# Performance work log

Hardware: AMD Instinct MI355X
Metric: run time of the kernel (lower is better)

Reference implementation:

```python
import jax, jax.numpy as jnp
import numpy as np

F_DIM = 128
N_RBF = 20
CUTOFF = 5.0
N_LAYERS = 3
EPS = 1e-8


def setup_inputs() -> dict:
    key = jax.random.key(0)
    ks = jax.random.split(key, 16)
    N, E = 10000, 320000
    atomic_numbers = jax.random.randint(ks[0], (N,), 0, 100)
    r_ij = jax.random.normal(ks[1], (E, 3), dtype=jnp.float32)
    idx_i = jnp.sort(jax.random.randint(ks[2], (E,), 0, N))
    idx_j = jax.random.randint(ks[3], (E,), 0, N)
    emb = jax.random.normal(ks[4], (100, F_DIM), dtype=jnp.float32)
    emb = emb.at[0].set(0.0)  # padding_idx=0
    s = 0.05
    return {
        "atomic_numbers": atomic_numbers,
        "r_ij": r_ij,
        "idx_i": idx_i,
        "idx_j": idx_j,
        "embedding": emb,
        "filt_W": jax.random.normal(ks[5], (N_RBF, N_LAYERS * 3 * F_DIM), dtype=jnp.float32) * s,
        "filt_b": jax.random.normal(ks[6], (N_LAYERS * 3 * F_DIM,), dtype=jnp.float32) * s,
        "int_W1": jax.random.normal(ks[7], (N_LAYERS, F_DIM, F_DIM), dtype=jnp.float32) * s,
        "int_b1": jax.random.normal(ks[8], (N_LAYERS, F_DIM), dtype=jnp.float32) * s,
        "int_W2": jax.random.normal(ks[9], (N_LAYERS, F_DIM, 3 * F_DIM), dtype=jnp.float32) * s,
        "int_b2": jax.random.normal(ks[10], (N_LAYERS, 3 * F_DIM), dtype=jnp.float32) * s,
        "mix_W1": jax.random.normal(ks[11], (N_LAYERS, 2 * F_DIM, F_DIM), dtype=jnp.float32) * s,
        "mix_b1": jax.random.normal(ks[12], (N_LAYERS, F_DIM), dtype=jnp.float32) * s,
        "mix_W2": jax.random.normal(ks[13], (N_LAYERS, F_DIM, 3 * F_DIM), dtype=jnp.float32) * s,
        "mix_b2": jax.random.normal(ks[14], (N_LAYERS, 3 * F_DIM), dtype=jnp.float32) * s,
        "mux_W": jax.random.normal(ks[15], (N_LAYERS, F_DIM, 2 * F_DIM), dtype=jnp.float32) * s,
    }


def _painn(embedding, filt_W, filt_b, int_W1, int_b1, int_W2, int_b2,
           mix_W1, mix_b1, mix_W2, mix_b2, mux_W,
           r_ij, atomic_numbers, idx_i, idx_j):
    N = atomic_numbers.shape[0]
    F = F_DIM
    d_ij = jnp.linalg.norm(r_ij, axis=1, keepdims=True)          # [E,1]
    dir_ij = r_ij / d_ij                                          # [E,3]
    # Gaussian RBF expansion
    offset = jnp.linspace(0.0, CUTOFF, N_RBF, dtype=jnp.float32)
    coeff = -0.5 / (offset[1] - offset[0]) ** 2
    phi = jnp.exp(coeff * (d_ij[..., None] - offset) ** 2)        # [E,1,n_rbf]
    # Cosine cutoff
    fcut = 0.5 * (jnp.cos(d_ij * jnp.pi / CUTOFF) + 1.0) * (d_ij < CUTOFF)  # [E,1]
    filters = (phi @ filt_W + filt_b) * fcut[..., None]           # [E,1,L*3F]
    filter_list = jnp.split(filters, N_LAYERS, axis=-1)

    q = embedding[atomic_numbers][:, None, :]                     # [N,1,F]
    mu = jnp.zeros((N, 3, F), dtype=q.dtype)

    for i in range(N_LAYERS):
        Wij = filter_list[i]                                      # [E,1,3F]
        # interaction
        h = jax.nn.silu(q @ int_W1[i] + int_b1[i])
        x = h @ int_W2[i] + int_b2[i]                             # [N,1,3F]
        xj = x[idx_j]                                             # [E,1,3F]
        muj = mu[idx_j]                                           # [E,3,F]
        xw = Wij * xj
        dq, dmuR, dmumu = jnp.split(xw, 3, axis=-1)               # each [E,1,F]
        dq = jax.ops.segment_sum(dq, idx_i, num_segments=N)       # [N,1,F]
        dmu = dmuR * dir_ij[:, :, None] + dmumu * muj             # [E,3,F]
        dmu = jax.ops.segment_sum(dmu, idx_i, num_segments=N)     # [N,3,F]
        q = q + dq
        mu = mu + dmu
        # mixing
        mu_mix = mu @ mux_W[i]                                    # [N,3,2F]
        mu_V, mu_W = jnp.split(mu_mix, 2, axis=-1)
        mu_Vn = jnp.sqrt(jnp.sum(mu_V ** 2, axis=-2, keepdims=True) + EPS)  # [N,1,F]
        ctx = jnp.concatenate([q, mu_Vn], axis=-1)                # [N,1,2F]
        h = jax.nn.silu(ctx @ mix_W1[i] + mix_b1[i])
        x = h @ mix_W2[i] + mix_b2[i]                             # [N,1,3F]
        dq_i, dmu_i, dqmu_i = jnp.split(x, 3, axis=-1)
        dmu_i = dmu_i * mu_W                                      # [N,3,F]
        dqmu_i = dqmu_i * jnp.sum(mu_V * mu_W, axis=1, keepdims=True)
        q = q + dq_i + dqmu_i
        mu = mu + dmu_i
    return q[:, 0, :], mu


def reference(atomic_numbers, r_ij, idx_i, idx_j, embedding, filt_W, filt_b,
              int_W1, int_b1, int_W2, int_b2, mix_W1, mix_b1, mix_W2, mix_b2, mux_W):
    return _painn(embedding, filt_W, filt_b, int_W1, int_b1, int_W2, int_b2,
                  mix_W1, mix_b1, mix_W2, mix_b2, mux_W,
                  r_ij, atomic_numbers, idx_i, idx_j)
```

## Files before the change

kernel.cpp:

```cpp
#include <hip/hip_runtime.h>
#include <hip/hip_bf16.h>
#include <hip/hip_fp16.h>

#define F_DIM 128
#define N_RBF 20
#define CUTOFF 5.0f
#define PI_F 3.14159265358979323846f
#define NPB 4

typedef float v2f __attribute__((ext_vector_type(2)));
typedef __attribute__((ext_vector_type(8))) short bf16x8;
typedef __attribute__((ext_vector_type(4))) float f32x4;
typedef _Float16 h2f __attribute__((ext_vector_type(2)));
typedef _Float16 f16x8 __attribute__((ext_vector_type(8)));

__device__ __forceinline__ unsigned int bf16_rtne(float f) {
    unsigned int u = __float_as_uint(f);
    u += 0x7fffu + ((u >> 16) & 1u);
    return u >> 16;
}
__device__ __forceinline__ unsigned int pack_bf2(float lo, float hi) {
    return bf16_rtne(lo) | (bf16_rtne(hi) << 16);
}
__device__ __forceinline__ float unpk_lo(unsigned int u) {
    return __uint_as_float(u << 16);
}
__device__ __forceinline__ float unpk_hi(unsigned int u) {
    return __uint_as_float(u & 0xffff0000u);
}
__device__ __forceinline__ float bf16_to_f(unsigned short s) {
    return __uint_as_float(((unsigned int)s) << 16);
}
__device__ __forceinline__ unsigned int pack_h2(float lo, float hi) {
    h2f h = (h2f){(_Float16)lo, (_Float16)hi};
    return __builtin_bit_cast(unsigned int, h);
}
__device__ __forceinline__ unsigned short f16_bits(float f) {
    _Float16 h = (_Float16)f;
    return __builtin_bit_cast(unsigned short, h);
}
__device__ __forceinline__ float f16_to_f(unsigned short s) {
    return (float)__builtin_bit_cast(_Float16, s);
}

__global__ __launch_bounds__(256) void k_pre(
        const int* __restrict__ idx_i, int* __restrict__ row_ptr,
        const float* __restrict__ r, unsigned int* __restrict__ geom,
        const float* __restrict__ muxW,
        const float* __restrict__ W1,
        const float* __restrict__ W2,
        const float* __restrict__ iW1,
        const float* __restrict__ iW2,
        const float* __restrict__ filt_W,
        const float* __restrict__ filt_b,
        unsigned short* __restrict__ muxWt,
        unsigned short* __restrict__ W1t,
        unsigned short* __restrict__ W2t,
        unsigned short* __restrict__ iW1t,
        unsigned short* __restrict__ iW2t,
        unsigned short* __restrict__ filtWt,
        int N, int E, int nbR, int nbG) {
    int bid = blockIdx.x;
    if (bid < nbR) {
        int i = bid * 256 + threadIdx.x;
        if (i > N) return;
        if (i == N) { row_ptr[N] = E; return; }
        int lo = 0, hi = E;
        while (lo < hi) {
            int mid = (lo + hi) >> 1;
            if (idx_i[mid] < i) lo = mid + 1; else hi = mid;
        }
        row_ptr[i] = lo;
        return;
    }
    if (bid < nbR + nbG) {
        int e = (bid - nbR) * 256 + threadIdx.x;
        if (e >= E) return;
        float x = r[e * 3], y = r[e * 3 + 1], z = r[e * 3 + 2];
        float d = sqrtf(x * x + y * y + z * z);
        float inv = 1.f / d;
        float fc = (d < CUTOFF) ? 0.5f * (__cosf(d * (PI_F / CUTOFF)) + 1.f) : 0.f;
        unsigned int* g = geom + (size_t)e * 16;
        float dx = x * inv, dy = y * inv, dz = z * inv;
        g[0] = __float_as_uint(dx);
        g[1] = __float_as_uint(dy);
        g[2] = __float_as_uint(dz);
        g[3] = __float_as_uint(fc);
        const float delta = CUTOFF / (N_RBF - 1);
        const float coeff = -0.5f / (delta * delta);
        float ph[N_RBF];
#pragma unroll
        for (int k = 0; k < N_RBF; k++) {
            float t = d - k * delta;
            ph[k] = __expf(coeff * t * t) * fc;
        }
#pragma unroll
        for (int k = 0; k < N_RBF / 2; k++)
            g[4 + k] = pack_h2(ph[2 * k], ph[2 * k + 1]);
        g[14] = pack_h2(fc, dx);
        g[15] = pack_h2(dy, dz);
        return;
    }
    int idx = (bid - nbR - nbG) * 256 + threadIdx.x;
    if (idx < 98304) {
        int l = idx / 32768, rem = idx % 32768;
        int c = rem / 128, k = rem % 128;
        muxWt[idx] = (unsigned short)bf16_rtne(muxW[l * 32768 + k * 256 + c]);
    } else if (idx < 196608) {
        int i2 = idx - 98304;
        int l = i2 / 32768, rem = i2 % 32768;
        int c = rem / 256, k = rem % 256;
        W1t[i2] = (unsigned short)bf16_rtne(W1[l * 32768 + k * 128 + c]);
    } else if (idx < 344064) {
        int i2 = idx - 196608;
        int l = i2 / 49152, rem = i2 % 49152;
        int c = rem / 128, k = rem % 128;
        W2t[i2] = (unsigned short)bf16_rtne(W2[l * 49152 + k * 384 + c]);
    } else if (idx < 393216) {
        int i2 = idx - 344064;
        int l = i2 / 16384, rem = i2 % 16384;
        int c = rem / 128, k = rem % 128;
        iW1t[i2] = (unsigned short)bf16_rtne(iW1[l * 16384 + k * 128 + c]);
    } else if (idx < 540672) {
        int i2 = idx - 393216;
        int l = i2 / 49152, rem = i2 % 49152;
        int c = rem / 128, k = rem % 128;
        iW2t[i2] = (unsigned short)bf16_rtne(iW2[l * 49152 + k * 384 + c]);
    } else if (idx < 568320) {
        int i2 = idx - 540672;
        int l = i2 / 9216, rem = i2 % 9216;
        int c = rem / 24, k = rem % 24;
        float v = 0.f;
        if (k < 20)       v = filt_W[k * 1152 + l * 384 + c];
        else if (k == 20) v = filt_b[l * 384 + c];
        _Float16 hv = (_Float16)v;
        filtWt[i2] = __builtin_bit_cast(unsigned short, hv);
    }
}

__global__ __launch_bounds__(256) void k_node_mfma(
        const int* __restrict__ Z,
        const float* __restrict__ emb,
        float* __restrict__ q,
        const unsigned short* __restrict__ iW1t,
        const float* __restrict__ b1,
        const unsigned short* __restrict__ iW2t,
        const float* __restrict__ b2,
        unsigned int* __restrict__ P, int N) {
    __shared__ unsigned short A[16 * 136];
    __shared__ unsigned short Ah[16 * 136];
    __shared__ float Xs[16 * 396];
    int t = threadIdx.x;
    int w = t >> 6, l = t & 63, quad = l >> 4, c0 = l & 15;
    int n0 = blockIdx.x * 16;

#pragma unroll
    for (int i = 0; i < 4; i++) {
        int flat = i * 256 + t;
        int node = flat >> 6, cp = flat & 63;
        int gn = n0 + node;
        unsigned int v = 0u;
        if (gn < N) {
            const float* s = emb + (size_t)Z[gn] * 128 + 2 * cp;
            float s0 = s[0], s1 = s[1];
            v = pack_bf2(s0, s1);
            float* qo = q + (size_t)gn * 128 + 2 * cp;
            qo[0] = s0; qo[1] = s1;
        }
        *(unsigned int*)&A[node * 136 + 2 * cp] = v;
    }
    __syncthreads();

    bf16x8 a1[4];
#pragma unroll
    for (int ks = 0; ks < 4; ks++)
        a1[ks] = *(const bf16x8*)&A[c0 * 136 + ks * 32 + quad * 8];
#pragma unroll
    for (int jj = 0; jj < 2; jj++) {
        int jg = 2 * w + jj;
        float bb = b1[16 * jg + c0];
        f32x4 acc = (f32x4){bb, bb, bb, bb};
#pragma unroll
        for (int ks = 0; ks < 4; ks++) {
            bf16x8 b = *(const bf16x8*)&iW1t[(16 * jg + c0) * 128 + ks * 32 + quad * 8];
            acc = __builtin_amdgcn_mfma_f32_16x16x32_bf16(a1[ks], b, acc, 0, 0, 0);
        }
#pragma unroll
        for (int r = 0; r < 4; r++) {
            float aa = acc[r];
            Ah[(quad * 4 + r) * 136 + 16 * jg + c0] =
                (unsigned short)bf16_rtne(aa / (1.f + __expf(-aa)));
        }
    }
    __syncthreads();

    bf16x8 a3[4];
#pragma unroll
    for (int ks = 0; ks < 4; ks++)
        a3[ks] = *(const bf16x8*)&Ah[c0 * 136 + ks * 32 + quad * 8];
#pragma unroll
    for (int jj = 0; jj < 6; jj++) {
        int jx = 6 * w + jj;
        float bb = b2[16 * jx + c0];
        f32x4 acc = (f32x4){bb, bb, bb, bb};
#pragma unroll
        for (int ks = 0; ks < 4; ks++) {
            bf16x8 b = *(const bf16x8*)&iW2t[(16 * jx + c0) * 128 + ks * 32 + quad * 8];
            acc = __builtin_amdgcn_mfma_f32_16x16x32_bf16(a3[ks], b, acc, 0, 0, 0);
        }
#pragma unroll
        for (int r = 0; r < 4; r++)
            Xs[(quad * 4 + r) * 396 + 16 * jx + c0] = acc[r];
    }
    __syncthreads();

    int n = t >> 4, fi = (t & 15) * 8;
    int gn = n0 + n;
    if (gn < N) {
        size_t base = (size_t)gn * 384;
        unsigned int d[8];
#pragma unroll
        for (int k = 0; k < 8; k++) {
            float x0 = Xs[n * 396 + fi + k];
            float x1 = Xs[n * 396 + 128 + fi + k];
            float x2 = Xs[n * 396 + 256 + fi + k];
            d[k] = pack_bf2(x0, x1);
            ((unsigned short*)&P[base + 256 + fi + k])[0] = (unsigned short)bf16_rtne(x2);
        }
        *(uint4*)&P[base + fi]     = make_uint4(d[0], d[1], d[2], d[3]);
        *(uint4*)&P[base + fi + 4] = make_uint4(d[4], d[5], d[6], d[7]);
    }
}

__device__ __forceinline__ f16x8 load_phi_frag(const unsigned int* __restrict__ geom,
                                               int ts, int c0, int quad, int E) {
    int ea = ts + c0;
    if (ea >= E) ea = E - 1;
    f16x8 a = {};
    if (quad < 3)
        a = *(const f16x8*)&geom[(size_t)ea * 16 + 4 + quad * 4];
    return a;
}

template <bool HAS_MU>
__global__ __launch_bounds__(256, 8) void k_edge(
        const unsigned int* __restrict__ P,
        const unsigned int* __restrict__ geom,
        const int* __restrict__ idx_j,
        const int* __restrict__ row_ptr,
        const unsigned short* __restrict__ filtWt,
        float* __restrict__ q,
        float* __restrict__ muD, int N, int E) {
    constexpr int NT = HAS_MU ? 6 : 4;
    constexpr int WS = HAS_MU ? 412 : 268;
    __shared__ unsigned short Ws[16 * WS];
    __shared__ float red[4][128];
    int t = threadIdx.x;
    int f = t & 127;
    int sub = __builtin_amdgcn_readfirstlane(t >> 7);
    int w = t >> 6, l = t & 63, quad = l >> 4, c0 = l & 15;

    f16x8 Bf[NT];
#pragma unroll
    for (int jj = 0; jj < NT; jj++) {
        int jx = NT * w + jj;
        f16x8 b = {};
        if (quad < 3)
            b = *(const f16x8*)&filtWt[(16 * jx + c0) * 24 + quad * 8];
        Bf[jj] = b;
    }

    int i0 = blockIdx.x * NPB;
    for (int nn = 0; nn < NPB; nn++) {
        int i = i0 + nn;
        if (i >= N) break;
        int rs = __builtin_amdgcn_readfirstlane(row_ptr[i]);
        int re = __builtin_amdgcn_readfirstlane(row_ptr[i + 1]);
        float dq = 0.f;
        v2f dm01 = (v2f){0.f, 0.f};
        float dm2 = 0.f;

        f16x8 a = load_phi_frag(geom, rs, c0, quad, E);
        for (int ts = rs; ts < re; ts += 16) {
#pragma unroll
            for (int jj = 0; jj < NT; jj++) {
                int jx = NT * w + jj;
                f32x4 acc = (f32x4){0.f, 0.f, 0.f, 0.f};
                acc = __builtin_amdgcn_mfma_f32_16x16x32_f16(a, Bf[jj], acc, 0, 0, 0);
#pragma unroll
                for (int r = 0; r < 4; r++)
                    Ws[(quad * 4 + r) * WS + 16 * jx + c0] = f16_bits(acc[r]);
            }
            __syncthreads();
            if (ts + 16 < re) a = load_phi_frag(geom, ts + 16, c0, quad, E);

            int te = (re < ts + 16) ? re : ts + 16;
            for (int e = ts + sub; e < te; e += 2) {
                int j = __builtin_amdgcn_readfirstlane(idx_j[e]);
                const unsigned int* Pj = P + (size_t)j * 384;
                unsigned int A = Pj[f];
                unsigned int B = 0, C = 0;
                if (HAS_MU) { B = Pj[128 + f]; C = Pj[256 + f]; }

                const float* g = (const float*)(geom + (size_t)e * 16);
                float dirx = g[0], diry = g[1], dirz = g[2];

                int eloc = e - ts;
                float wq = f16_to_f(Ws[eloc * WS + f]);
                float wr = f16_to_f(Ws[eloc * WS + 128 + f]);

                float xq = unpk_lo(A), xr = unpk_hi(A);
                dq += wq * xq;
                float s_r = wr * xr;
                if (HAS_MU) {
                    float wm = f16_to_f(Ws[eloc * WS + 256 + f]);
                    float xm = unpk_lo(C);
                    float s_m = wm * xm;
                    dm01 += (v2f){s_r, s_r} * (v2f){dirx, diry} +
                            (v2f){s_m, s_m} * (v2f){unpk_lo(B), unpk_hi(B)};
                    dm2  += s_r * dirz + s_m * unpk_hi(C);
                } else {
                    dm01 += (v2f){s_r, s_r} * (v2f){dirx, diry};
                    dm2  += s_r * dirz;
                }
            }
            __syncthreads();
        }

        if (sub == 1) { red[0][f] = dq; red[1][f] = dm01.x; red[2][f] = dm01.y; red[3][f] = dm2; }
        __syncthreads();
        if (sub == 0) {
            dq += red[0][f];
            float d0 = dm01.x + red[1][f], d1 = dm01.y + red[2][f];
            dm2 += red[3][f];
            q[(size_t)i * 128 + f] += dq;
            size_t base = (size_t)i * 384;
            if (HAS_MU) {
                muD[base + f]       += d0;
                muD[base + 128 + f] += d1;
                muD[base + 256 + f] += dm2;
            } else {
                muD[base + f]       = d0;
                muD[base + 128 + f] = d1;
                muD[base + 256 + f] = dm2;
            }
        }
        __syncthreads();
    }
}

__global__ __launch_bounds__(256, 3) void k_mix_fused(
        float* __restrict__ q, float* __restrict__ mu,
        const unsigned short* __restrict__ muxWt,
        const unsigned short* __restrict__ W1t,
        const unsigned short* __restrict__ W2t,
        const float* __restrict__ b1,
        const float* __restrict__ b2,
        const unsigned short* __restrict__ niW1t,
        const float* __restrict__ nib1,
        const unsigned short* __restrict__ niW2t,
        const float* __restrict__ nib2,
        int has_node,
        unsigned int* __restrict__ P, int N) {
    constexpr int XS = 516;
    __shared__ __align__(16) unsigned char LDSm[54144];
    unsigned short* A   = (unsigned short*)LDSm;
    unsigned short* Wsp = (unsigned short*)(LDSm + 8448);
    float*          Xs  = (float*)(LDSm + 21120);
    unsigned short* Amu = (unsigned short*)(LDSm + 21120);

    int t = threadIdx.x;
    int w = t >> 6, l = t & 63, quad = l >> 4, c0 = l & 15;
    int n0 = blockIdx.x * 16;

#pragma unroll
    for (int i = 0; i < 4; i++) {
        int flat = i * 256 + t;
        int node = flat >> 6, cp = flat & 63, gn = n0 + node;
        unsigned int v = 0u;
        if (gn < N) { const float* s = q + (size_t)gn * 128 + 2 * cp; v = pack_bf2(s[0], s[1]); }
        *(unsigned int*)&A[node * 264 + 2 * cp] = v;
    }
#pragma unroll
    for (int i = 0; i < 12; i++) {
        int flat = i * 256 + t;
        int row = flat >> 6, cp = flat & 63;
        int node = row & 15, c = row >> 4, gn = n0 + node;
        unsigned int v = 0u;
        if (gn < N) {
            const float* s = mu + (size_t)gn * 384 + c * 128 + 2 * cp;
            v = pack_bf2(s[0], s[1]);
        }
        *(unsigned int*)&Amu[row * 136 + 2 * cp] = v;
    }
    __syncthreads();

    f32x4 vn2[2], S[2];
#pragma unroll
    for (int jj = 0; jj < 2; jj++) { vn2[jj] = (f32x4){0,0,0,0}; S[jj] = (f32x4){0,0,0,0}; }
#pragma unroll
    for (int rt = 0; rt < 3; rt++) {
        bf16x8 af[4];
#pragma unroll
        for (int ks = 0; ks < 4; ks++)
            af[ks] = *(const bf16x8*)&Amu[(rt * 16 + c0) * 136 + ks * 32 + quad * 8];
#pragma unroll
        for (int jj = 0; jj < 2; jj++) {
            int jv = 2 * w + jj;
            f32x4 V = (f32x4){0,0,0,0}, Wm = (f32x4){0,0,0,0};
#pragma unroll
            for (int ks = 0; ks < 4; ks++) {
                bf16x8 bV = *(const bf16x8*)&muxWt[(16 * jv + c0) * 128 + ks * 32 + quad * 8];
                V = __builtin_amdgcn_mfma_f32_16x16x32_bf16(af[ks], bV, V, 0, 0, 0);
            }
#pragma unroll
            for (int ks = 0; ks < 4; ks++) {
                bf16x8 bW = *(const bf16x8*)&muxWt[(16 * (jv + 8) + c0) * 128 + ks * 32 + quad * 8];
                Wm = __builtin_amdgcn_mfma_f32_16x16x32_bf16(af[ks], bW, Wm, 0, 0, 0);
            }
            vn2[jj] += V * V;
            S[jj]   += V * Wm;
#pragma unroll
            for (int r = 0; r < 4; r++)
                Wsp[rt * 2112 + (quad * 4 + r) * 132 + 16 * jv + c0] =
                    (unsigned short)bf16_rtne(Wm[r]);
        }
    }
#pragma unroll
    for (int jj = 0; jj < 2; jj++) {
        int jv = 2 * w + jj;
#pragma unroll
        for (int r = 0; r < 4; r++)
            A[(quad * 4 + r) * 264 + 128 + 16 * jv + c0] =
                (unsigned short)bf16_rtne(sqrtf(vn2[jj][r] + 1e-8f));
    }
    __syncthreads();

    bf16x8 a2[8];
#pragma unroll
    for (int ks = 0; ks < 8; ks++)
        a2[ks] = *(const bf16x8*)&A[c0 * 264 + ks * 32 + quad * 8];
    {
        unsigned short htmp[2][4];
#pragma unroll
        for (int jj = 0; jj < 2; jj++) {
            int jg = 2 * w + jj;
            float bb = b1[16 * jg + c0];
            f32x4 acc = (f32x4){bb, bb, bb, bb};
#pragma unroll
            for (int ks = 0; ks < 8; ks++) {
                bf16x8 b = *(const bf16x8*)&W1t[(16 * jg + c0) * 256 + ks * 32 + quad * 8];
                acc = __builtin_amdgcn_mfma_f32_16x16x32_bf16(a2[ks], b, acc, 0, 0, 0);
            }
#pragma unroll
            for (int r = 0; r < 4; r++) {
                float aa = acc[r];
                htmp[jj][r] = (unsigned short)bf16_rtne(aa / (1.f + __expf(-aa)));
            }
        }
        __syncthreads();
#pragma unroll
        for (int jj = 0; jj < 2; jj++) {
            int jg = 2 * w + jj;
#pragma unroll
            for (int r = 0; r < 4; r++)
                A[(quad * 4 + r) * 264 + 128 + 16 * jg + c0] = htmp[jj][r];
        }
    }
    __syncthreads();

    bf16x8 a3[4];
#pragma unroll
    for (int ks = 0; ks < 4; ks++)
        a3[ks] = *(const bf16x8*)&A[c0 * 264 + 128 + ks * 32 + quad * 8];
#pragma unroll
    for (int jj = 0; jj < 6; jj++) {
        int jx = 6 * w + jj;
        float bb = b2[16 * jx + c0];
        f32x4 acc = (f32x4){bb, bb, bb, bb};
#pragma unroll
        for (int ks = 0; ks < 4; ks++) {
            bf16x8 b = *(const bf16x8*)&W2t[(16 * jx + c0) * 128 + ks * 32 + quad * 8];
            acc = __builtin_amdgcn_mfma_f32_16x16x32_bf16(a3[ks], b, acc, 0, 0, 0);
        }
#pragma unroll
        for (int r = 0; r < 4; r++)
            Xs[(quad * 4 + r) * XS + 16 * jx + c0] = acc[r];
    }
#pragma unroll
    for (int jj = 0; jj < 2; jj++) {
        int jv = 2 * w + jj;
#pragma unroll
        for (int r = 0; r < 4; r++)
            Xs[(quad * 4 + r) * XS + 388 + 16 * jv + c0] = S[jj][r];
    }
    __syncthreads();

    int n = t >> 4, fi = (t & 15) * 8;
    int gn = n0 + n;
    if (gn < N) {
        float* qp = q + (size_t)gn * 128 + fi;
        float qn[8];
#pragma unroll
        for (int k = 0; k < 8; k++) {
            qn[k] = qp[k] + Xs[n * XS + fi + k] +
                    Xs[n * XS + 256 + fi + k] * Xs[n * XS + 388 + fi + k];
            qp[k] = qn[k];
        }
        unsigned int qd[4];
#pragma unroll
        for (int p = 0; p < 4; p++) qd[p] = pack_bf2(qn[2 * p], qn[2 * p + 1]);
        *(uint4*)&A[n * 264 + fi] = make_uint4(qd[0], qd[1], qd[2], qd[3]);

        size_t base = (size_t)gn * 384;
        float m[3][8];
#pragma unroll
        for (int c = 0; c < 3; c++) {
            float* mp = mu + base + c * 128 + fi;
#pragma unroll
            for (int k = 0; k < 8; k++) {
                m[c][k] = mp[k] + Xs[n * XS + 128 + fi + k] *
                                  bf16_to_f(Wsp[c * 2112 + n * 132 + fi + k]);
                mp[k] = m[c][k];
            }
        }
        unsigned int d[8];
#pragma unroll
        for (int k = 0; k < 8; k++) {
            d[k] = pack_bf2(m[0][k], m[1][k]);
            ((unsigned short*)&P[base + 256 + fi + k])[1] = (unsigned short)bf16_rtne(m[2][k]);
        }
        *(uint4*)&P[base + 128 + fi]     = make_uint4(d[0], d[1], d[2], d[3]);
        *(uint4*)&P[base + 128 + fi + 4] = make_uint4(d[4], d[5], d[6], d[7]);
    }
    __syncthreads();

    if (has_node) {
        unsigned short* Ah = Wsp;
        bf16x8 a1[4];
#pragma unroll
        for (int ks = 0; ks < 4; ks++)
            a1[ks] = *(const bf16x8*)&A[c0 * 264 + ks * 32 + quad * 8];
#pragma unroll
        for (int jj = 0; jj < 2; jj++) {
            int jg = 2 * w + jj;
            float bb = nib1[16 * jg + c0];
            f32x4 acc = (f32x4){bb, bb, bb, bb};
#pragma unroll
            for (int ks = 0; ks < 4; ks++) {
                bf16x8 b = *(const bf16x8*)&niW1t[(16 * jg + c0) * 128 + ks * 32 + quad * 8];
                acc = __builtin_amdgcn_mfma_f32_16x16x32_bf16(a1[ks], b, acc, 0, 0, 0);
            }
#pragma unroll
            for (int r = 0; r < 4; r++) {
                float aa = acc[r];
                Ah[(quad * 4 + r) * 136 + 16 * jg + c0] =
                    (unsigned short)bf16_rtne(aa / (1.f + __expf(-aa)));
            }
        }
        __syncthreads();

        bf16x8 a4[4];
#pragma unroll
        for (int ks = 0; ks < 4; ks++)
            a4[ks] = *(const bf16x8*)&Ah[c0 * 136 + ks * 32 + quad * 8];
#pragma unroll
        for (int jj = 0; jj < 6; jj++) {
            int jx = 6 * w + jj;
            float bb = nib2[16 * jx + c0];
            f32x4 acc = (f32x4){bb, bb, bb, bb};
#pragma unroll
            for (int ks = 0; ks < 4; ks++) {
                bf16x8 b = *(const bf16x8*)&niW2t[(16 * jx + c0) * 128 + ks * 32 + quad * 8];
                acc = __builtin_amdgcn_mfma_f32_16x16x32_bf16(a4[ks], b, acc, 0, 0, 0);
            }
#pragma unroll
            for (int r = 0; r < 4; r++)
                Xs[(quad * 4 + r) * XS + 16 * jx + c0] = acc[r];
        }
        __syncthreads();

        if (gn < N) {
            size_t base = (size_t)gn * 384;
            unsigned int d[8];
#pragma unroll
            for (int k = 0; k < 8; k++) {
                float x0 = Xs[n * XS + fi + k];
                float x1 = Xs[n * XS + 128 + fi + k];
                float x2 = Xs[n * XS + 256 + fi + k];
                d[k] = pack_bf2(x0, x1);
                ((unsigned short*)&P[base + 256 + fi + k])[0] = (unsigned short)bf16_rtne(x2);
            }
            *(uint4*)&P[base + fi]     = make_uint4(d[0], d[1], d[2], d[3]);
            *(uint4*)&P[base + fi + 4] = make_uint4(d[4], d[5], d[6], d[7]);
        }
    }
}

extern "C" void kernel_launch(void* const* d_in, const int* in_sizes, int n_in,
                              void* d_out, int out_size, void* d_ws, size_t ws_size,
                              hipStream_t stream) {
    const int*   Z      = (const int*)d_in[0];
    const float* r_ij   = (const float*)d_in[1];
    const int*   idx_i  = (const int*)d_in[2];
    const int*   idx_j  = (const int*)d_in[3];
    const float* emb    = (const float*)d_in[4];
    const float* filt_W = (const float*)d_in[5];
    const float* filt_b = (const float*)d_in[6];
    const float* int_W1 = (const float*)d_in[7];
    const float* int_b1 = (const float*)d_in[8];
    const float* int_W2 = (const float*)d_in[9];
    const float* int_b2 = (const float*)d_in[10];
    const float* mix_W1 = (const float*)d_in[11];
    const float* mix_b1 = (const float*)d_in[12];
    const float* mix_W2 = (const float*)d_in[13];
    const float* mix_b2 = (const float*)d_in[14];
    const float* mux_W  = (const float*)d_in[15];

    int N = in_sizes[0];
    int E = in_sizes[2];

    float* q   = (float*)d_out;
    float* muD = q + (size_t)N * 128;

    unsigned int* geom = (unsigned int*)d_ws;
    unsigned int* P = geom + (size_t)E * 16;
    int* row_ptr = (int*)(P + (size_t)N * 384);
    uintptr_t waddr = (uintptr_t)(row_ptr + N + 1);
    waddr = (waddr + 15) & ~(uintptr_t)15;
    unsigned short* muxWt = (unsigned short*)waddr;
    unsigned short* W1t   = muxWt + 98304;
    unsigned short* W2t   = W1t + 98304;
    unsigned short* iW1t  = W2t + 147456;
    unsigned short* iW2t  = iW1t + 49152;
    unsigned short* filtWt = iW2t + 147456;

    int nbR = (N + 1 + 255) / 256;
    int nbG = (E + 255) / 256;
    k_pre<<<nbR + nbG + 2220, 256, 0, stream>>>(
        idx_i, row_ptr, r_ij, geom,
        mux_W, mix_W1, mix_W2, int_W1, int_W2, filt_W, filt_b,
        muxWt, W1t, W2t, iW1t, iW2t, filtWt, N, E, nbR, nbG);

    int tiles = (N + 15) / 16;
    k_node_mfma<<<tiles, 256, 0, stream>>>(
        Z, emb, q, iW1t, int_b1, iW2t, int_b2, P, N);
    for (int l = 0; l < 3; l++) {
        if (l == 0)
            k_edge<false><<<(N + NPB - 1) / NPB, 256, 0, stream>>>(
                P, geom, idx_j, row_ptr, filtWt, q, muD, N, E);
        else
            k_edge<true><<<(N + NPB - 1) / NPB, 256, 0, stream>>>(
                P, geom, idx_j, row_ptr, filtWt + (size_t)l * 9216, q, muD, N, E);
        int nl = (l < 2) ? (l + 1) : 0;
        k_mix_fused<<<tiles, 256, 0, stream>>>(
            q, muD, muxWt + (size_t)l * 32768, W1t + (size_t)l * 32768,
            W2t + (size_t)l * 49152, mix_b1 + l * 128, mix_b2 + l * 384,
            iW1t + (size_t)nl * 16384, int_b1 + nl * 128,
            iW2t + (size_t)nl * 49152, int_b2 + nl * 384,
            (l < 2) ? 1 : 0, P, N);
    }
}
```

Measured before the change: 532.6 us.

## Prefetch next edge tile's neighbor features into registers in edge kernel

The edge kernel now loads the idx_j values for a whole 16-edge tile with one vector load and broadcasts them with readlane. The neighbor rows of P for the next tile are gathered into registers while the current tile is being processed, so those gathers overlap with compute. The inner edge loop is fully unrolled over 8 slots with masking instead of a variable-trip loop. Occupancy bound drops from 8 to 6 to make room for the extra registers, and the mix kernel skips writing packed mu into P on the last layer where it is no longer read.

After: 880.6 us. 1.65x slower.

```diff
diff --git a/kernel.cpp b/kernel.cpp
--- a/kernel.cpp
+++ b/kernel.cpp
@@ -243,7 +243,7 @@
 }
 
 template <bool HAS_MU>
-__global__ __launch_bounds__(256, 8) void k_edge(
+__global__ __launch_bounds__(256, 6) void k_edge(
         const unsigned int* __restrict__ P,
         const unsigned int* __restrict__ geom,
         const int* __restrict__ idx_j,
@@ -259,6 +259,7 @@
     int f = t & 127;
     int sub = __builtin_amdgcn_readfirstlane(t >> 7);
     int w = t >> 6, l = t & 63, quad = l >> 4, c0 = l & 15;
+    int ll8 = l & 7;
 
     f16x8 Bf[NT];
 #pragma unroll
@@ -271,78 +272,101 @@
     }
 
     int i0 = blockIdx.x * NPB;
+    int Rs = __builtin_amdgcn_readfirstlane(row_ptr[i0]);
+
+    unsigned int PA[8], PB[8], PC[8];
+    f16x8 aF = load_phi_frag(geom, Rs, c0, quad, E);
+    {
+        int ea0 = Rs + 2 * ll8 + sub; if (ea0 > E - 1) ea0 = E - 1;
+        int idxv = idx_j[ea0];
+#pragma unroll
+        for (int k = 0; k < 8; k++) {
+            int j = __builtin_amdgcn_readlane(idxv, k);
+            const unsigned int* Pj = P + (size_t)j * 384;
+            PA[k] = Pj[f];
+            if (HAS_MU) { PB[k] = Pj[128 + f]; PC[k] = Pj[256 + f]; }
+        }
+    }
+
     for (int nn = 0; nn < NPB; nn++) {
         int i = i0 + nn;
         if (i >= N) break;
         int rs = __builtin_amdgcn_readfirstlane(row_ptr[i]);
         int re = __builtin_amdgcn_readfirstlane(row_ptr[i + 1]);
-        float dq = 0.f;
-        v2f dm01 = (v2f){0.f, 0.f};
-        float dm2 = 0.f;
-
-        f16x8 a = load_phi_frag(geom, rs, c0, quad, E);
+        float dq = 0.f, dm0 = 0.f, dm1 = 0.f, dm2 = 0.f;
+
         for (int ts = rs; ts < re; ts += 16) {
 #pragma unroll
             for (int jj = 0; jj < NT; jj++) {
                 int jx = NT * w + jj;
                 f32x4 acc = (f32x4){0.f, 0.f, 0.f, 0.f};
-                acc = __builtin_amdgcn_mfma_f32_16x16x32_f16(a, Bf[jj], acc, 0, 0, 0);
+                acc = __builtin_amdgcn_mfma_f32_16x16x32_f16(aF, Bf[jj], acc, 0, 0, 0);
 #pragma unroll
                 for (int r = 0; r < 4; r++)
                     Ws[(quad * 4 + r) * WS + 16 * jx + c0] = f16_bits(acc[r]);
             }
+            int nts = (ts + 16 < re) ? ts + 16 : re;
+            f16x8 aN = load_phi_frag(geom, nts, c0, quad, E);
+            int eaN = nts + 2 * ll8 + sub; if (eaN > E - 1) eaN = E - 1;
+            int idxvN = idx_j[eaN];
             __syncthreads();
-            if (ts + 16 < re) a = load_phi_frag(geom, ts + 16, c0, quad, E);
-
-            int te = (re < ts + 16) ? re : ts + 16;
-            for (int e = ts + sub; e < te; e += 2) {
-                int j = __builtin_amdgcn_readfirstlane(idx_j[e]);
-                const unsigned int* Pj = P + (size_t)j * 384;
-                unsigned int A = Pj[f];
-                unsigned int B = 0, C = 0;
-                if (HAS_MU) { B = Pj[128 + f]; C = Pj[256 + f]; }
-
-                const float* g = (const float*)(geom + (size_t)e * 16);
+
+            int nv = re - ts; if (nv > 16) nv = 16;
+#pragma unroll
+            for (int k = 0; k < 8; k++) {
+                int eloc = 2 * k + sub;
+                float msk = (eloc < nv) ? 1.f : 0.f;
+                int ee = ts + eloc; if (ee > E - 1) ee = E - 1;
+                const float* g = (const float*)(geom + (size_t)ee * 16);
                 float dirx = g[0], diry = g[1], dirz = g[2];
 
-                int eloc = e - ts;
-                float wq = f16_to_f(Ws[eloc * WS + f]);
-                float wr = f16_to_f(Ws[eloc * WS + 128 + f]);
-
+                float wq = f16_to_f(Ws[eloc * WS + f]) * msk;
+                float wr = f16_to_f(Ws[eloc * WS + 128 + f]) * msk;
+
+                unsigned int A = PA[k];
                 float xq = unpk_lo(A), xr = unpk_hi(A);
                 dq += wq * xq;
                 float s_r = wr * xr;
                 if (HAS_MU) {
-                    float wm = f16_to_f(Ws[eloc * WS + 256 + f]);
-                    float xm = unpk_lo(C);
-                    float s_m = wm * xm;
-                    dm01 += (v2f){s_r, s_r} * (v2f){dirx, diry} +
-                            (v2f){s_m, s_m} * (v2f){unpk_lo(B), unpk_hi(B)};
-                    dm2  += s_r * dirz + s_m * unpk_hi(C);
+                    float wm = f16_to_f(Ws[eloc * WS + 256 + f]) * msk;
+                    unsigned int B = PB[k], C = PC[k];
+                    float s_m = wm * unpk_lo(C);
+                    dm0 += s_r * dirx + s_m * unpk_lo(B);
+                    dm1 += s_r * diry + s_m * unpk_hi(B);
+                    dm2 += s_r * dirz + s_m * unpk_hi(C);
                 } else {
-                    dm01 += (v2f){s_r, s_r} * (v2f){dirx, diry};
-                    dm2  += s_r * dirz;
+                    dm0 += s_r * dirx;
+                    dm1 += s_r * diry;
+                    dm2 += s_r * dirz;
                 }
             }
+#pragma unroll
+            for (int k = 0; k < 8; k++) {
+                int j = __builtin_amdgcn_readlane(idxvN, k);
+                const unsigned int* Pj = P + (size_t)j * 384;
+                PA[k] = Pj[f];
+                if (HAS_MU) { PB[k] = Pj[128 + f]; PC[k] = Pj[256 + f]; }
+            }
+            aF = aN;
             __syncthreads();
         }
 
-        if (sub == 1) { red[0][f] = dq; red[1][f] = dm01.x; red[2][f] = dm01.y; red[3][f] = dm2; }
+        if (sub == 1) { red[0][f] = dq; red[1][f] = dm0; red[2][f] = dm1; red[3][f] = dm2; }
         __syncthreads();
         if (sub == 0) {
-            dq += red[0][f];
-            float d0 = dm01.x + red[1][f], d1 = dm01.y + red[2][f];
-            dm2 += red[3][f];
+            dq  += red[0][f];
+            float d0 = dm0 + red[1][f], d1 = dm1 + red[2][f];
+            float d2 = dm2 + red[3][f];
             q[(size_t)i * 128 + f] += dq;
             size_t base = (size_t)i * 384;
             if (HAS_MU) {
                 muD[base + f]       += d0;
                 muD[base + 128 + f] += d1;
-                muD[base + 256 + f] += dm2;
+                muD[base + 256 + f] += d2;
             } else {
                 muD[base + f]       = d0;
                 muD[base + 128 + f] = d1;
-                muD[base + 256 + f] = dm2;
+                muD[base + 256 + f] = d2;
             }
         }
         __syncthreads();
@@ -524,14 +548,16 @@
                 mp[k] = m[c][k];
             }
         }
-        unsigned int d[8];
-#pragma unroll
-        for (int k = 0; k < 8; k++) {
-            d[k] = pack_bf2(m[0][k], m[1][k]);
-            ((unsigned short*)&P[base + 256 + fi + k])[1] = (unsigned short)bf16_rtne(m[2][k]);
-        }
-        *(uint4*)&P[base + 128 + fi]     = make_uint4(d[0], d[1], d[2], d[3]);
-        *(uint4*)&P[base + 128 + fi + 4] = make_uint4(d[4], d[5], d[6], d[7]);
+        if (has_node) {
+            unsigned int d[8];
+#pragma unroll
+            for (int k = 0; k < 8; k++) {
+                d[k] = pack_bf2(m[0][k], m[1][k]);
+                ((unsigned short*)&P[base + 256 + fi + k])[1] = (unsigned short)bf16_rtne(m[2][k]);
+            }
+            *(uint4*)&P[base + 128 + fi]     = make_uint4(d[0], d[1], d[2], d[3]);
+            *(uint4*)&P[base + 128 + fi + 4] = make_uint4(d[4], d[5], d[6], d[7]);
+        }
     }
     __syncthreads();
 
```
